# Kernel tuning notes

Hardware: AMD Instinct MI355X
Metric: run time of the kernel (lower is better)

## Reference

```python
import jax, jax.numpy as jnp
import numpy as np

T, D, F, FS, E = 2048, 1024, 2048, 2048, 8
TOP_K = 1


def setup_inputs() -> dict:
    key = jax.random.key(0)
    ks = jax.random.split(key, 8)
    sd = 1.0 / np.sqrt(D)
    sf = 1.0 / np.sqrt(F)
    sfs = 1.0 / np.sqrt(FS)
    return {
        "hidden_states": jax.random.normal(ks[0], (T, D), jnp.float32),
        "router_w": jax.random.normal(ks[1], (E, D), jnp.float32) * sd,     # Linear(D->E), no bias
        "w_gate": jax.random.normal(ks[2], (E, D, F), jnp.float32) * sd,    # fused gate half
        "w_up": jax.random.normal(ks[3], (E, D, F), jnp.float32) * sd,      # fused up half
        "w_down": jax.random.normal(ks[4], (E, F, D), jnp.float32) * sf,
        "ws_gate": jax.random.normal(ks[5], (D, FS), jnp.float32) * sd,
        "ws_up": jax.random.normal(ks[6], (D, FS), jnp.float32) * sd,
        "ws_down": jax.random.normal(ks[7], (FS, D), jnp.float32) * sfs,
    }


def reference(hidden_states, router_w, w_gate, w_up, w_down, ws_gate, ws_up, ws_down):
    # Router: logits -> top-k -> sigmoid of top-k values (Llama4RenormalizeMoeRoutingMethod)
    logits = hidden_states @ router_w.T                      # [T, E]
    top_vals, top_idx = jax.lax.top_k(logits, TOP_K)         # [T, K]
    scores = jax.nn.sigmoid(top_vals.astype(jnp.float32)).astype(hidden_states.dtype)
    # Combine weights [T, E]; apply_router_weight_on_input=True -> scale INPUT per routed copy
    combine = (jax.nn.one_hot(top_idx, E, dtype=hidden_states.dtype) * scores[..., None]).sum(axis=1)
    xe = combine.T[:, :, None] * hidden_states[None]          # [E, T, D] (zero for non-routed tokens)
    g = jnp.einsum('etd,edf->etf', xe, w_gate)
    u = jnp.einsum('etd,edf->etf', xe, w_up)
    routed = jnp.einsum('etf,efd->etd', jax.nn.silu(g) * u, w_down).sum(axis=0)  # [T, D]
    # Shared expert (GatedMLP, SiLU)
    shared = (jax.nn.silu(hidden_states @ ws_gate) * (hidden_states @ ws_up)) @ ws_down
    return shared + routed
```

## Files before the change

kernel.cpp:

```cpp
#include <hip/hip_runtime.h>
#include <hip/hip_bf16.h>
#include <cstdint>
#include <cstddef>

#define T_TOK 2048
#define DIM   1024
#define FDIM  2048
#define NEXP  8

#define GU_MAX 48
#define DN_MAX 96

typedef short  short8  __attribute__((ext_vector_type(8)));
typedef float  floatx4 __attribute__((ext_vector_type(4)));

__device__ inline unsigned short f2bf(float f) {
    unsigned int u = __builtin_bit_cast(unsigned int, f);
    unsigned int r = (u + 0x7FFFu + ((u >> 16) & 1u)) >> 16;
    return (unsigned short)r;
}

__device__ inline unsigned int cvtpk(float a, float b) {
    unsigned int r;
    asm("v_cvt_pk_bf16_f32 %0, %1, %2" : "=v"(r) : "v"(a), "v"(b));
    return r;
}

__device__ inline void glds16(const void* g, const unsigned short* lds_base, int elem_off) {
    int u = __builtin_amdgcn_readfirstlane(elem_off);
    __builtin_amdgcn_global_load_lds(
        (const __attribute__((address_space(1))) unsigned int*)g,
        (__attribute__((address_space(3))) unsigned int*)(lds_base + u), 16, 0, 0);
}

__global__ __launch_bounds__(256) void k_router(
    const float* __restrict__ h, const float* __restrict__ rw,
    int* __restrict__ counts, int* __restrict__ lists,
    unsigned short* __restrict__ hb, unsigned short* __restrict__ xb)
{
    int w = threadIdx.x >> 6, lane = threadIdx.x & 63;
    int t = blockIdx.x * 4 + w;
    const float* hrow = h + (size_t)t * DIM;
    float hv[16];
    #pragma unroll
    for (int i = 0; i < 16; ++i) hv[i] = hrow[lane + 64 * i];
    float acc[NEXP];
    #pragma unroll
    for (int e = 0; e < NEXP; ++e) {
        const float* r = rw + (size_t)e * DIM;
        float s = 0.f;
        #pragma unroll
        for (int i = 0; i < 16; ++i) s += hv[i] * r[lane + 64 * i];
        acc[e] = s;
    }
    #pragma unroll
    for (int e = 0; e < NEXP; ++e) {
        float s = acc[e];
        for (int off = 32; off > 0; off >>= 1) s += __shfl_down(s, off);
        acc[e] = s;
    }
    float score = 0.f;
    if (lane == 0) {
        int be = 0; float bv = acc[0];
        #pragma unroll
        for (int e = 1; e < NEXP; ++e) if (acc[e] > bv) { bv = acc[e]; be = e; }
        score = 1.f / (1.f + __expf(-bv));
        int pos = atomicAdd(&counts[be], 1);
        lists[be * T_TOK + pos] = t;
    }
    score = __shfl(score, 0);
    unsigned short* hbr = hb + (size_t)t * DIM;
    unsigned short* xbr = xb + (size_t)t * DIM;
    #pragma unroll
    for (int i = 0; i < 16; ++i) {
        hbr[lane + 64 * i] = f2bf(hv[i]);
        xbr[lane + 64 * i] = f2bf(score * hv[i]);
    }
}

__global__ void k_schedule(const int* __restrict__ counts,
                           int* __restrict__ gu, int* __restrict__ dn)
{
    if (threadIdx.x != 0 || blockIdx.x != 0) return;
    int n = 0;
    for (int e = 0; e < NEXP; ++e) {
        int c = counts[e];
        for (int r = 0; r < c; r += 128) gu[n++] = (e << 16) | r;
    }
    for (int r = 0; r < T_TOK; r += 128) gu[n++] = (NEXP << 16) | r;
    while (n < GU_MAX) gu[n++] = -1;
    n = 0;
    for (int e = 0; e < NEXP; ++e) {
        int c = counts[e];
        for (int r = 0; r < c; r += 128)
            for (int kc = 0; kc < 4; ++kc)
                dn[n++] = (kc << 26) | (e << 16) | r;
    }
    while (n < DN_MAX) dn[n++] = -1;
}

__global__ __launch_bounds__(256, 2) void k_gateup(
    const unsigned short* __restrict__ xb, const unsigned short* __restrict__ hb,
    const float* __restrict__ w_gate, const float* __restrict__ w_up,
    const float* __restrict__ ws_gate, const float* __restrict__ ws_up,
    const int* __restrict__ counts, const int* __restrict__ lists,
    const int* __restrict__ gu_tiles, unsigned short* __restrict__ Hc)
{
    int ent = gu_tiles[blockIdx.y];
    if (ent < 0) return;
    int e = ent >> 16, row0 = ent & 0xffff;
    bool sh = (e == NEXP);
    int cnt = sh ? T_TOK : counts[e];
    const unsigned short* Asrc = sh ? hb : xb;
    const float* Bg = sh ? ws_gate : w_gate + (size_t)e * DIM * FDIM;
    const float* Bu = sh ? ws_up   : w_up   + (size_t)e * DIM * FDIM;
    int outoff = sh ? FDIM : 0;
    int col0 = blockIdx.x * 64;

    __shared__ int toks[128];
    __shared__ __align__(16) unsigned short As [2][128 * 32];
    __shared__ __align__(16) unsigned short Bgs[2][64 * 32];
    __shared__ __align__(16) unsigned short Bus[2][64 * 32];

    int tid = threadIdx.x;
    if (tid < 128) {
        int r = row0 + tid;
        toks[tid] = (r < cnt) ? (sh ? r : lists[e * T_TOK + r]) : -1;
    }
    __syncthreads();

    int lane = tid & 63, w = tid >> 6;

    size_t agoff[2]; int albase[2];
    #pragma unroll
    for (int it = 0; it < 2; ++it) {
        int tt = tid + it * 256;
        int rr = tt >> 2, sq = tt & 3;
        int kg = (sq ^ ((rr >> 1) & 3)) * 8;
        int tk = toks[rr]; if (tk < 0) tk = 0;
        agoff[it] = (size_t)tk * DIM + kg;
        albase[it] = (it * 256 + w * 64) * 8;
    }

    int c = tid & 63;
    int slotW = (w ^ ((c >> 1) & 3)) * 8;
    const float* bgp = Bg + (size_t)(w * 8) * FDIM + col0 + c;
    const float* bup = Bu + (size_t)(w * 8) * FDIM + col0 + c;

    float gx[8], ux[8];
    auto loadB = [&](int k0) {
        const float* pg = bgp + (size_t)k0 * FDIM;
        const float* pu = bup + (size_t)k0 * FDIM;
        #pragma unroll
        for (int j = 0; j < 8; ++j) {
            gx[j] = pg[(size_t)j * FDIM];
            ux[j] = pu[(size_t)j * FDIM];
        }
    };
    auto commitB = [&](int p_) {
        unsigned int gw[4], uw[4];
        #pragma unroll
        for (int j = 0; j < 4; ++j) {
            gw[j] = cvtpk(gx[2*j], gx[2*j+1]);
            uw[j] = cvtpk(ux[2*j], ux[2*j+1]);
        }
        *(uint4*)&Bgs[p_][c * 32 + slotW] = make_uint4(gw[0], gw[1], gw[2], gw[3]);
        *(uint4*)&Bus[p_][c * 32 + slotW] = make_uint4(uw[0], uw[1], uw[2], uw[3]);
    };
    auto loadA = [&](int k0, int p_) {
        #pragma unroll
        for (int it = 0; it < 2; ++it)
            glds16(Asrc + agoff[it] + k0, &As[p_][0], albase[it]);
    };

    floatx4 accg[2][4], accu[2][4];
    #pragma unroll
    for (int mi = 0; mi < 2; ++mi)
    #pragma unroll
    for (int ni = 0; ni < 4; ++ni) {
        floatx4 z = {0.f, 0.f, 0.f, 0.f};
        accg[mi][ni] = z; accu[mi][ni] = z;
    }

    loadA(0, 0);
    loadB(0);
    commitB(0);
    loadB(32);

    int p = 0;
    for (int k0 = 0; k0 < DIM; k0 += 32) {
        asm volatile("s_waitcnt vmcnt(16) lgkmcnt(0)\n\ts_barrier" ::: "memory");
        bool more = (k0 + 32 < DIM);
        if (more) loadA(k0 + 32, p ^ 1);
        __builtin_amdgcn_sched_barrier(0);
        int g = lane >> 4;
        short8 af[2], bgf[4], buf_[4];
        #pragma unroll
        for (int mi = 0; mi < 2; ++mi) {
            int r = w * 32 + mi * 16 + (lane & 15);
            int slot = (g ^ ((r >> 1) & 3)) * 8;
            af[mi] = *(const short8*)&As[p][r * 32 + slot];
        }
        #pragma unroll
        for (int ni = 0; ni < 4; ++ni) {
            int n = ni * 16 + (lane & 15);
            int slot = (g ^ ((n >> 1) & 3)) * 8;
            bgf[ni]  = *(const short8*)&Bgs[p][n * 32 + slot];
            buf_[ni] = *(const short8*)&Bus[p][n * 32 + slot];
        }
        if (more) {
            commitB(p ^ 1);
            int nk2 = k0 + 64; if (nk2 >= DIM) nk2 = 0;
            loadB(nk2);
        }
        __builtin_amdgcn_s_setprio(1);
        #pragma unroll
        for (int mi = 0; mi < 2; ++mi)
        #pragma unroll
        for (int ni = 0; ni < 4; ++ni) {
            accg[mi][ni] = __builtin_amdgcn_mfma_f32_16x16x32_bf16(af[mi], bgf[ni],  accg[mi][ni], 0, 0, 0);
            accu[mi][ni] = __builtin_amdgcn_mfma_f32_16x16x32_bf16(af[mi], buf_[ni], accu[mi][ni], 0, 0, 0);
        }
        __builtin_amdgcn_s_setprio(0);
        p ^= 1;
    }

    #pragma unroll
    for (int mi = 0; mi < 2; ++mi)
    #pragma unroll
    for (int ni = 0; ni < 4; ++ni)
    #pragma unroll
    for (int r = 0; r < 4; ++r) {
        int row = w * 32 + mi * 16 + (lane >> 4) * 4 + r;
        int tok = toks[row];
        if (tok < 0) continue;
        int col = col0 + ni * 16 + (lane & 15);
        float gv = accg[mi][ni][r], uv = accu[mi][ni][r];
        float hval = (gv / (1.f + __expf(-gv))) * uv;
        Hc[(size_t)tok * (2 * FDIM) + outoff + col] = f2bf(hval);
    }
}

__global__ __launch_bounds__(256, 2) void k_down(
    const unsigned short* __restrict__ Hc,
    const float* __restrict__ w_down, const float* __restrict__ ws_down,
    const int* __restrict__ counts, const int* __restrict__ lists,
    const int* __restrict__ dn_tiles, float* __restrict__ out)
{
    int ent = dn_tiles[blockIdx.y];
    if (ent < 0) return;
    int kc = (ent >> 26) & 3, e = (ent >> 16) & 0xff, row0 = ent & 0xffff;
    int half = kc >> 1, chunk = kc & 1;
    int cnt = counts[e];
    const float* B = (half ? ws_down : w_down + (size_t)e * FDIM * DIM)
                     + (size_t)(chunk * 1024) * DIM;
    int col0 = blockIdx.x * 64;
    size_t abase = (size_t)(half * FDIM + chunk * 1024);

    __shared__ int toks[128];
    __shared__ __align__(16) unsigned short As[2][128 * 32];
    __shared__ __align__(16) unsigned short Bs[2][64 * 32];

    int tid = threadIdx.x;
    if (tid < 128) {
        int r = row0 + tid;
        toks[tid] = (r < cnt) ? lists[e * T_TOK + r] : -1;
    }
    __syncthreads();

    int lane = tid & 63, w = tid >> 6;

    size_t agoff[2]; int albase[2];
    #pragma unroll
    for (int it = 0; it < 2; ++it) {
        int tt = tid + it * 256;
        int rr = tt >> 2, sq = tt & 3;
        int kg = (sq ^ ((rr >> 1) & 3)) * 8;
        int tk = toks[rr]; if (tk < 0) tk = 0;
        agoff[it] = (size_t)tk * (2 * FDIM) + abase + kg;
        albase[it] = (it * 256 + w * 64) * 8;
    }

    int c = tid & 63;
    int slotW = (w ^ ((c >> 1) & 3)) * 8;
    const float* bp_ = B + (size_t)(w * 8) * DIM + col0 + c;

    float bx[8];
    auto loadB = [&](int k0) {
        const float* pb = bp_ + (size_t)k0 * DIM;
        #pragma unroll
        for (int j = 0; j < 8; ++j) bx[j] = pb[(size_t)j * DIM];
    };
    auto commitB = [&](int p_) {
        unsigned int bw[4];
        #pragma unroll
        for (int j = 0; j < 4; ++j) bw[j] = cvtpk(bx[2*j], bx[2*j+1]);
        *(uint4*)&Bs[p_][c * 32 + slotW] = make_uint4(bw[0], bw[1], bw[2], bw[3]);
    };
    auto loadA = [&](int k0, int p_) {
        #pragma unroll
        for (int it = 0; it < 2; ++it)
            glds16(Hc + agoff[it] + k0, &As[p_][0], albase[it]);
    };

    floatx4 acc[2][4];
    #pragma unroll
    for (int mi = 0; mi < 2; ++mi)
    #pragma unroll
    for (int ni = 0; ni < 4; ++ni) {
        floatx4 z = {0.f, 0.f, 0.f, 0.f};
        acc[mi][ni] = z;
    }

    loadA(0, 0);
    loadB(0);
    commitB(0);
    loadB(32);

    int p = 0;
    for (int k0 = 0; k0 < 1024; k0 += 32) {
        asm volatile("s_waitcnt vmcnt(8) lgkmcnt(0)\n\ts_barrier" ::: "memory");
        bool more = (k0 + 32 < 1024);
        if (more) loadA(k0 + 32, p ^ 1);
        __builtin_amdgcn_sched_barrier(0);
        int g = lane >> 4;
        short8 af[2], bf[4];
        #pragma unroll
        for (int mi = 0; mi < 2; ++mi) {
            int r = w * 32 + mi * 16 + (lane & 15);
            int slot = (g ^ ((r >> 1) & 3)) * 8;
            af[mi] = *(const short8*)&As[p][r * 32 + slot];
        }
        #pragma unroll
        for (int ni = 0; ni < 4; ++ni) {
            int n = ni * 16 + (lane & 15);
            int slot = (g ^ ((n >> 1) & 3)) * 8;
            bf[ni] = *(const short8*)&Bs[p][n * 32 + slot];
        }
        if (more) {
            commitB(p ^ 1);
            int nk2 = k0 + 64; if (nk2 >= 1024) nk2 = 0;
            loadB(nk2);
        }
        __builtin_amdgcn_s_setprio(1);
        #pragma unroll
        for (int mi = 0; mi < 2; ++mi)
        #pragma unroll
        for (int ni = 0; ni < 4; ++ni)
            acc[mi][ni] = __builtin_amdgcn_mfma_f32_16x16x32_bf16(af[mi], bf[ni], acc[mi][ni], 0, 0, 0);
        __builtin_amdgcn_s_setprio(0);
        p ^= 1;
    }

    #pragma unroll
    for (int mi = 0; mi < 2; ++mi)
    #pragma unroll
    for (int ni = 0; ni < 4; ++ni)
    #pragma unroll
    for (int r = 0; r < 4; ++r) {
        int row = w * 32 + mi * 16 + (lane >> 4) * 4 + r;
        int tok = toks[row];
        if (tok < 0) continue;
        int col = col0 + ni * 16 + (lane & 15);
        atomicAdd(&out[(size_t)tok * DIM + col], acc[mi][ni][r]);
    }
}

extern "C" void kernel_launch(void* const* d_in, const int* in_sizes, int n_in,
                              void* d_out, int out_size, void* d_ws, size_t ws_size,
                              hipStream_t stream)
{
    const float* h   = (const float*)d_in[0];
    const float* rw  = (const float*)d_in[1];
    const float* wg  = (const float*)d_in[2];
    const float* wu  = (const float*)d_in[3];
    const float* wd  = (const float*)d_in[4];
    const float* wsg = (const float*)d_in[5];
    const float* wsu = (const float*)d_in[6];
    const float* wsd = (const float*)d_in[7];
    float* out = (float*)d_out;

    char* ws = (char*)d_ws;
    int* counts   = (int*)ws;
    int* gu_tiles = (int*)(ws + 256);
    int* dn_tiles = (int*)(ws + 1024);
    int* lists    = (int*)(ws + 2048);
    unsigned short* hb = (unsigned short*)(ws + 131072);
    unsigned short* xb = hb + (size_t)T_TOK * DIM;
    unsigned short* Hc = xb + (size_t)T_TOK * DIM;

    (void)hipMemsetAsync(counts, 0, 64, stream);
    (void)hipMemsetAsync(out, 0, (size_t)T_TOK * DIM * sizeof(float), stream);
    k_router<<<dim3(T_TOK / 4), 256, 0, stream>>>(h, rw, counts, lists, hb, xb);
    k_schedule<<<dim3(1), 64, 0, stream>>>(counts, gu_tiles, dn_tiles);
    k_gateup<<<dim3(FDIM / 64, GU_MAX), 256, 0, stream>>>(
        xb, hb, wg, wu, wsg, wsu, counts, lists, gu_tiles, Hc);
    k_down<<<dim3(DIM / 64, DN_MAX), 256, 0, stream>>>(
        Hc, wd, wsd, counts, lists, dn_tiles, out);
}
```

Measured before the change: 372.9 us.

## Triple-buffer A tiles and move B commit after MFMAs in both GEMM kernels

Both the gate/up and down kernels now keep three LDS stages for the A (activation) tile, prefetching two k-steps ahead, and the waitcnt thresholds are raised to match. The B register-to-LDS commit and the next B global load are moved from before the MFMA block to after it. The aim is more latency hiding for the gathered A loads and keeping the MFMAs from waiting on the B conversion. The cost is extra LDS per block, which may lower occupancy, and some risk from the hand-tuned vmcnt counts.

```diff
diff --git a/kernel.cpp b/kernel.cpp
--- a/kernel.cpp
+++ b/kernel.cpp
@@ -118,7 +118,7 @@
     int col0 = blockIdx.x * 64;
 
     __shared__ int toks[128];
-    __shared__ __align__(16) unsigned short As [2][128 * 32];
+    __shared__ __align__(16) unsigned short As [3 * 128 * 32];
     __shared__ __align__(16) unsigned short Bgs[2][64 * 32];
     __shared__ __align__(16) unsigned short Bus[2][64 * 32];
 
@@ -167,10 +167,10 @@
         *(uint4*)&Bgs[p_][c * 32 + slotW] = make_uint4(gw[0], gw[1], gw[2], gw[3]);
         *(uint4*)&Bus[p_][c * 32 + slotW] = make_uint4(uw[0], uw[1], uw[2], uw[3]);
     };
-    auto loadA = [&](int k0, int p_) {
+    auto loadA = [&](int k0, int aoff) {
         #pragma unroll
         for (int it = 0; it < 2; ++it)
-            glds16(Asrc + agoff[it] + k0, &As[p_][0], albase[it]);
+            glds16(Asrc + agoff[it] + k0, &As[0], aoff + albase[it]);
     };
 
     floatx4 accg[2][4], accu[2][4];
@@ -183,35 +183,31 @@
     }
 
     loadA(0, 0);
+    loadA(32, 4096);
     loadB(0);
     commitB(0);
     loadB(32);
 
-    int p = 0;
+    int g = lane >> 4, l15 = lane & 15;
+    int acur = 0, an1 = 4096, an2 = 8192;
+    int pb = 0;
     for (int k0 = 0; k0 < DIM; k0 += 32) {
-        asm volatile("s_waitcnt vmcnt(16) lgkmcnt(0)\n\ts_barrier" ::: "memory");
-        bool more = (k0 + 32 < DIM);
-        if (more) loadA(k0 + 32, p ^ 1);
+        asm volatile("s_waitcnt vmcnt(18) lgkmcnt(0)\n\ts_barrier" ::: "memory");
+        if (k0 + 64 < DIM) loadA(k0 + 64, an2);
         __builtin_amdgcn_sched_barrier(0);
-        int g = lane >> 4;
         short8 af[2], bgf[4], buf_[4];
         #pragma unroll
         for (int mi = 0; mi < 2; ++mi) {
-            int r = w * 32 + mi * 16 + (lane & 15);
+            int r = w * 32 + mi * 16 + l15;
             int slot = (g ^ ((r >> 1) & 3)) * 8;
-            af[mi] = *(const short8*)&As[p][r * 32 + slot];
+            af[mi] = *(const short8*)&As[acur + r * 32 + slot];
         }
         #pragma unroll
         for (int ni = 0; ni < 4; ++ni) {
-            int n = ni * 16 + (lane & 15);
+            int n = ni * 16 + l15;
             int slot = (g ^ ((n >> 1) & 3)) * 8;
-            bgf[ni]  = *(const short8*)&Bgs[p][n * 32 + slot];
-            buf_[ni] = *(const short8*)&Bus[p][n * 32 + slot];
-        }
-        if (more) {
-            commitB(p ^ 1);
-            int nk2 = k0 + 64; if (nk2 >= DIM) nk2 = 0;
-            loadB(nk2);
+            bgf[ni]  = *(const short8*)&Bgs[pb][n * 32 + slot];
+            buf_[ni] = *(const short8*)&Bus[pb][n * 32 + slot];
         }
         __builtin_amdgcn_s_setprio(1);
         #pragma unroll
@@ -222,7 +218,12 @@
             accu[mi][ni] = __builtin_amdgcn_mfma_f32_16x16x32_bf16(af[mi], buf_[ni], accu[mi][ni], 0, 0, 0);
         }
         __builtin_amdgcn_s_setprio(0);
-        p ^= 1;
+        if (k0 + 32 < DIM) {
+            commitB(pb ^ 1);
+            if (k0 + 64 < DIM) loadB(k0 + 64);
+        }
+        int tmp = acur; acur = an1; an1 = an2; an2 = tmp;
+        pb ^= 1;
     }
 
     #pragma unroll
@@ -258,7 +259,7 @@
     size_t abase = (size_t)(half * FDIM + chunk * 1024);
 
     __shared__ int toks[128];
-    __shared__ __align__(16) unsigned short As[2][128 * 32];
+    __shared__ __align__(16) unsigned short As[3 * 128 * 32];
     __shared__ __align__(16) unsigned short Bs[2][64 * 32];
 
     int tid = threadIdx.x;
@@ -297,10 +298,10 @@
         for (int j = 0; j < 4; ++j) bw[j] = cvtpk(bx[2*j], bx[2*j+1]);
         *(uint4*)&Bs[p_][c * 32 + slotW] = make_uint4(bw[0], bw[1], bw[2], bw[3]);
     };
-    auto loadA = [&](int k0, int p_) {
+    auto loadA = [&](int k0, int aoff) {
         #pragma unroll
         for (int it = 0; it < 2; ++it)
-            glds16(Hc + agoff[it] + k0, &As[p_][0], albase[it]);
+            glds16(Hc + agoff[it] + k0, &As[0], aoff + albase[it]);
     };
 
     floatx4 acc[2][4];
@@ -313,34 +314,30 @@
     }
 
     loadA(0, 0);
+    loadA(32, 4096);
     loadB(0);
     commitB(0);
     loadB(32);
 
-    int p = 0;
+    int g = lane >> 4, l15 = lane & 15;
+    int acur = 0, an1 = 4096, an2 = 8192;
+    int pb = 0;
     for (int k0 = 0; k0 < 1024; k0 += 32) {
-        asm volatile("s_waitcnt vmcnt(8) lgkmcnt(0)\n\ts_barrier" ::: "memory");
-        bool more = (k0 + 32 < 1024);
-        if (more) loadA(k0 + 32, p ^ 1);
+        asm volatile("s_waitcnt vmcnt(10) lgkmcnt(0)\n\ts_barrier" ::: "memory");
+        if (k0 + 64 < 1024) loadA(k0 + 64, an2);
         __builtin_amdgcn_sched_barrier(0);
-        int g = lane >> 4;
         short8 af[2], bf[4];
         #pragma unroll
         for (int mi = 0; mi < 2; ++mi) {
-            int r = w * 32 + mi * 16 + (lane & 15);
+            int r = w * 32 + mi * 16 + l15;
             int slot = (g ^ ((r >> 1) & 3)) * 8;
-            af[mi] = *(const short8*)&As[p][r * 32 + slot];
+            af[mi] = *(const short8*)&As[acur + r * 32 + slot];
         }
         #pragma unroll
         for (int ni = 0; ni < 4; ++ni) {
-            int n = ni * 16 + (lane & 15);
+            int n = ni * 16 + l15;
             int slot = (g ^ ((n >> 1) & 3)) * 8;
-            bf[ni] = *(const short8*)&Bs[p][n * 32 + slot];
-        }
-        if (more) {
-            commitB(p ^ 1);
-            int nk2 = k0 + 64; if (nk2 >= 1024) nk2 = 0;
-            loadB(nk2);
+            bf[ni] = *(const short8*)&Bs[pb][n * 32 + slot];
         }
         __builtin_amdgcn_s_setprio(1);
         #pragma unroll
@@ -349,7 +346,12 @@
         for (int ni = 0; ni < 4; ++ni)
             acc[mi][ni] = __builtin_amdgcn_mfma_f32_16x16x32_bf16(af[mi], bf[ni], acc[mi][ni], 0, 0, 0);
         __builtin_amdgcn_s_setprio(0);
-        p ^= 1;
+        if (k0 + 32 < 1024) {
+            commitB(pb ^ 1);
+            if (k0 + 64 < 1024) loadB(k0 + 64);
+        }
+        int tmp = acur; acur = an1; an1 = an2; an2 = tmp;
+        pb ^= 1;
     }
 
     #pragma unroll
```

Result: no change. 379.7 us (+1.8%).
